# Optimization experiments

Hardware: AMD Instinct MI355X
Metric: run time of the kernel (lower is better)

Reference implementation:

```python
import jax, jax.numpy as jnp
import numpy as np

HIDDEN = 1024
HEADS = 16
CHUNK = 128
NEG_INF = -1e10  # matches source's -10000000000.0


def setup_inputs() -> dict:
    key = jax.random.key(0)
    k1, k2, k3 = jax.random.split(key, 3)
    B, S = 2, 4096
    x = jax.random.normal(k1, (B, S, HIDDEN), dtype=jnp.float32)
    w_qkv = jax.random.normal(k2, (HIDDEN, 3 * HIDDEN), dtype=jnp.float32) / np.sqrt(HIDDEN).astype(np.float32)
    w_out = jax.random.normal(k3, (HIDDEN, HIDDEN), dtype=jnp.float32) / np.sqrt(HIDDEN).astype(np.float32)
    return {"x": x, "w_qkv": w_qkv, "w_out": w_out}


def reference(x, w_qkv, w_out):
    B, S, _ = x.shape
    H, D = HEADS, HIDDEN // HEADS
    # fused qkv projection (flax Dense, no bias): [B,S,3,H,D]
    qkv = (x @ w_qkv).reshape(B, S, 3, H, D)
    q, k, v = qkv[:, :, 0], qkv[:, :, 1], qkv[:, :, 2]
    scale = jnp.sqrt(jnp.asarray(D, x.dtype))
    n_chunks = S // CHUNK
    # [n_chunks, B, CHUNK, H, D] query chunks; scan keeps only one chunk's
    # [B,H,CHUNK,S] score tensor live at a time (faithful to source's chunking).
    q_chunks = q.reshape(B, n_chunks, CHUNK, H, D).transpose(1, 0, 2, 3, 4)
    starts = jnp.arange(n_chunks) * CHUNK

    def step(carry, inp):
        qc, start = inp  # qc: [B,CHUNK,H,D]
        scores = jnp.einsum('bqhd,bkhd->bhqk', qc, k) / scale  # [B,H,CHUNK,S]
        causal = (jnp.arange(CHUNK)[:, None] + start) >= jnp.arange(S)[None, :]
        scores = jnp.where(causal[None, None], scores, NEG_INF)
        attn = jax.nn.softmax(scores, axis=-1)
        out_c = jnp.einsum('bhqk,bkhd->bqhd', attn, v).reshape(B, CHUNK, H * D)
        return carry, out_c

    _, outs = jax.lax.scan(step, None, (q_chunks, starts))  # [n,B,CHUNK,hidden]
    out = outs.transpose(1, 0, 2, 3).reshape(B, S, H * D)
    return out @ w_out
```

## Files before the change

kernel.cpp:

```cpp
#include <hip/hip_runtime.h>
#include <hip/hip_bf16.h>

#define SEQ 4096
#define BATCH 2
#define HEADS 16
#define DHEAD 64
#define HID 1024

typedef unsigned short ushort_t;
typedef unsigned int uint_t;
typedef __attribute__((ext_vector_type(8))) short short8;
typedef __attribute__((ext_vector_type(4))) float f32x4;
typedef __attribute__((ext_vector_type(16))) float f32x16;
typedef __attribute__((ext_vector_type(4))) uint_t u32x4;

__device__ __forceinline__ float exp2_fast(float x) {
  return __builtin_amdgcn_exp2f(x);
}

__device__ __forceinline__ float max3f(float a, float b, float c) {
  float r;
  asm("v_max3_f32 %0, %1, %2, %3" : "=v"(r) : "v"(a), "v"(b), "v"(c));
  return r;
}

__device__ __forceinline__ ushort_t f2b(float f) {
  unsigned u = __builtin_bit_cast(unsigned, f);
  unsigned r = 0x7fffu + ((u >> 16) & 1u);
  return (ushort_t)((u + r) >> 16);
}

__device__ __forceinline__ uint_t cvt_pk_bf16(float lo, float hi) {
  uint_t r;
  asm("v_cvt_pk_bf16_f32 %0, %1, %2" : "=v"(r) : "v"(lo), "v"(hi));
  return r;
}

__device__ __forceinline__ void permlane_swap(uint_t& a, uint_t& b) {
  asm("v_permlane32_swap_b32 %0, %1" : "+v"(a), "+v"(b));
}

__device__ __forceinline__ void gload16(const void* g, void* l) {
  __builtin_amdgcn_global_load_lds((const __attribute__((address_space(1))) void*)g,
                                   (__attribute__((address_space(3))) void*)l, 16, 0, 0);
}

__device__ __forceinline__ f32x4 mfma_bf16(short8 a, short8 b, f32x4 c) {
  return __builtin_amdgcn_mfma_f32_16x16x32_bf16(a, b, c, 0, 0, 0);
}

__device__ __forceinline__ f32x16 mfma32_bf16(short8 a, short8 b, f32x16 c) {
  return __builtin_amdgcn_mfma_f32_32x32x16_bf16(a, b, c, 0, 0, 0);
}

__global__ void cvt_kernel(const float* __restrict__ in, ushort_t* __restrict__ out, int n4) {
  int i = blockIdx.x * blockDim.x + threadIdx.x;
  if (i >= n4) return;
  float4 v = reinterpret_cast<const float4*>(in)[i];
  ushort4 o;
  o.x = f2b(v.x); o.y = f2b(v.y); o.z = f2b(v.z); o.w = f2b(v.w);
  reinterpret_cast<ushort4*>(out)[i] = o;
}

__global__ void transpose_cvt_kernel(const float* __restrict__ in, ushort_t* __restrict__ out,
                                     int rows, int cols) {
  __shared__ float tile[32][33];
  int tx = threadIdx.x & 31, ty = threadIdx.x >> 5;
  int r0 = blockIdx.y * 32, c0 = blockIdx.x * 32;
#pragma unroll
  for (int i = 0; i < 32; i += 8)
    tile[ty + i][tx] = in[(size_t)(r0 + ty + i) * cols + c0 + tx];
  __syncthreads();
#pragma unroll
  for (int i = 0; i < 32; i += 8)
    out[(size_t)(c0 + ty + i) * rows + r0 + tx] = f2b(tile[tx][ty + i]);
}

template <int MODE>
__global__ __launch_bounds__(256, 2)
void gemm_kernel(const ushort_t* __restrict__ A, const ushort_t* __restrict__ BT,
                 int M, int N, int K,
                 ushort_t* __restrict__ qg, ushort_t* __restrict__ kg,
                 ushort_t* __restrict__ vTg, float* __restrict__ outf) {
  __shared__ ushort_t lA[128 * 64];
  __shared__ ushort_t lB[128 * 64];
  int tid = threadIdx.x;
  int lane = tid & 63, w = tid >> 6;
  int m0 = blockIdx.x * 128, n0 = blockIdx.y * 128;
  int wr = (w >> 1) * 64, wc = (w & 1) * 64;
  int lr = lane & 15, lg = lane >> 4;

  const f32x4 z4 = {0.f, 0.f, 0.f, 0.f};
  f32x4 acc[4][4];
#pragma unroll
  for (int m = 0; m < 4; ++m)
#pragma unroll
    for (int n = 0; n < 4; ++n) acc[m][n] = z4;

  int ktiles = K >> 6;
  for (int kt = 0; kt < ktiles; ++kt) {
    int k0 = kt << 6;
#pragma unroll
    for (int i = 0; i < 4; ++i) {
      int c = i * 256 + tid;
      int row = c >> 3, cc = c & 7;
      gload16(A + (size_t)(m0 + row) * K + k0 + (cc ^ (row & 7)) * 8, lA + c * 8);
    }
#pragma unroll
    for (int i = 0; i < 4; ++i) {
      int c = i * 256 + tid;
      int row = c >> 3, cc = c & 7;
      gload16(BT + (size_t)(n0 + row) * K + k0 + (cc ^ (row & 7)) * 8, lB + c * 8);
    }
    __syncthreads();
#pragma unroll
    for (int kk = 0; kk < 2; ++kk) {
      short8 a[4], b[4];
#pragma unroll
      for (int m = 0; m < 4; ++m) {
        int row = wr + m * 16 + lr, cc = kk * 4 + lg;
        a[m] = *(const short8*)(lA + row * 64 + ((cc ^ (row & 7)) << 3));
      }
#pragma unroll
      for (int n = 0; n < 4; ++n) {
        int row = wc + n * 16 + lr, cc = kk * 4 + lg;
        b[n] = *(const short8*)(lB + row * 64 + ((cc ^ (row & 7)) << 3));
      }
      __builtin_amdgcn_s_setprio(1);
#pragma unroll
      for (int m = 0; m < 4; ++m)
#pragma unroll
        for (int n = 0; n < 4; ++n)
          acc[m][n] = mfma_bf16(a[m], b[n], acc[m][n]);
      __builtin_amdgcn_s_setprio(0);
    }
    __syncthreads();
  }

#pragma unroll
  for (int m = 0; m < 4; ++m)
#pragma unroll
    for (int n = 0; n < 4; ++n)
#pragma unroll
      for (int r = 0; r < 4; ++r) {
        int i = m0 + wr + m * 16 + lg * 4 + r;
        int j = n0 + wc + n * 16 + lr;
        float v = acc[m][n][r];
        if (MODE == 0) {
          int mat = j >> 10, rem = j & 1023;
          int h = rem >> 6, d = rem & 63;
          int b = i >> 12, s = i & 4095;
          int bh = b * HEADS + h;
          ushort_t val = f2b(mat == 0 ? v * 0.18033688f : v);
          if (mat == 0)      qg[((size_t)bh * SEQ + s) * DHEAD + d] = val;
          else if (mat == 1) kg[((size_t)bh * SEQ + s) * DHEAD + d] = val;
          else               vTg[((size_t)bh * DHEAD + d) * SEQ + s] = val;
        } else {
          outf[(size_t)i * N + j] = v;
        }
      }
}

struct QS {
  short8 qf[4];
  f32x16 o[2];
  float mrow, lsum;
};

__device__ __forceinline__ void attn_tile(int diag, int w, int l31, int hi, int lane,
                                          const ushort_t* lKc, const ushort_t* lVc, QS& st) {
  f32x16 s[4];
#pragma unroll
  for (int t = 0; t < 4; ++t)
#pragma unroll
    for (int r = 0; r < 16; ++r) s[t][r] = 0.f;

#pragma unroll
  for (int t = 0; t < 4; ++t) {
    int row = t * 32 + l31;
#pragma unroll
    for (int kb = 0; kb < 4; ++kb) {
      int cc = kb * 2 + hi;
      short8 kf = *(const short8*)(lKc + row * 64 + ((cc ^ (row & 7)) << 3));
      __builtin_amdgcn_s_setprio(1);
      s[t] = mfma32_bf16(kf, st.qf[kb], s[t]);
      __builtin_amdgcn_s_setprio(0);
    }
  }

  if (diag) {
    int q = w * 32 + l31;
#pragma unroll
    for (int t = 0; t < 4; ++t)
#pragma unroll
      for (int r = 0; r < 16; ++r)
        if (t * 32 + (r & 3) + 8 * (r >> 2) + 4 * hi > q) s[t][r] = -1e30f;
  }

  float mx = fmaxf(s[0][0], s[0][1]);
#pragma unroll
  for (int t = 0; t < 4; ++t)
#pragma unroll
    for (int r = (t == 0 ? 2 : 0); r < 16; r += 2)
      mx = max3f(mx, s[t][r], s[t][r + 1]);
  mx = fmaxf(mx, __shfl_xor(mx, 32));
  float mo = st.mrow;
  if (!__all(mx - mo <= 8.0f)) {
    float mn = fmaxf(mo, mx);
    float al = exp2_fast(mo - mn);
    st.mrow = mn;
    st.lsum *= al;
#pragma unroll
    for (int r = 0; r < 16; ++r) {
      float alo = __shfl(al, (r & 3) + 8 * (r >> 2) + 4 * hi);
      st.o[0][r] *= alo;
      st.o[1][r] *= alo;
    }
  }
  float mloc = st.mrow;
  float rsv[4];
#pragma unroll
  for (int t = 0; t < 4; ++t) {
    float a = 0.f;
#pragma unroll
    for (int r = 0; r < 16; ++r) {
      float p = exp2_fast(s[t][r] - mloc);
      s[t][r] = p;
      a += p;
    }
    rsv[t] = a;
  }
  float rs = (rsv[0] + rsv[1]) + (rsv[2] + rsv[3]);
  rs += __shfl_xor(rs, 32);
  st.lsum += rs;

  short8 pa[8];
#pragma unroll
  for (int t = 0; t < 4; ++t) {
    uint_t w0 = cvt_pk_bf16(s[t][0], s[t][1]);
    uint_t w1 = cvt_pk_bf16(s[t][2], s[t][3]);
    uint_t w2 = cvt_pk_bf16(s[t][4], s[t][5]);
    uint_t w3 = cvt_pk_bf16(s[t][6], s[t][7]);
    permlane_swap(w0, w2);
    permlane_swap(w1, w3);
    u32x4 f0 = {w0, w1, w2, w3};
    pa[2 * t] = __builtin_bit_cast(short8, f0);
    uint_t w4 = cvt_pk_bf16(s[t][8], s[t][9]);
    uint_t w5 = cvt_pk_bf16(s[t][10], s[t][11]);
    uint_t w6 = cvt_pk_bf16(s[t][12], s[t][13]);
    uint_t w7 = cvt_pk_bf16(s[t][14], s[t][15]);
    permlane_swap(w4, w6);
    permlane_swap(w5, w7);
    u32x4 f1 = {w4, w5, w6, w7};
    pa[2 * t + 1] = __builtin_bit_cast(short8, f1);
  }

#pragma unroll
  for (int nd = 0; nd < 2; ++nd) {
    int row = nd * 32 + l31;
#pragma unroll
    for (int kb = 0; kb < 8; ++kb) {
      int cc = kb * 2 + hi;
      short8 vf = *(const short8*)(lVc + row * 128 + ((cc ^ (row & 15)) << 3));
      __builtin_amdgcn_s_setprio(1);
      st.o[nd] = mfma32_bf16(pa[kb], vf, st.o[nd]);
      __builtin_amdgcn_s_setprio(0);
    }
  }
}

__device__ __forceinline__ void attn_epilogue(const QS& st, int q0, int bh,
                                              int w, int l31, int hi,
                                              ushort_t* __restrict__ og) {
  int b = bh >> 4, h = bh & 15;
#pragma unroll
  for (int r = 0; r < 16; ++r) {
    int qr = (r & 3) + 8 * (r >> 2) + 4 * hi;
    float ls = __shfl(st.lsum, qr);
    float inv = 1.0f / ls;
    int srow = q0 + w * 32 + qr;
#pragma unroll
    for (int nd = 0; nd < 2; ++nd) {
      int col = h * 64 + nd * 32 + l31;
      og[((size_t)b * SEQ + srow) * HID + col] = f2b(st.o[nd][r] * inv);
    }
  }
}

__global__ __launch_bounds__(256, 2)
void attn_kernel(const ushort_t* __restrict__ qg, const ushort_t* __restrict__ kg,
                 const ushort_t* __restrict__ vTg, ushort_t* __restrict__ og) {
  __shared__ ushort_t lK[2][128 * 64];
  __shared__ ushort_t lV[2][64 * 128];

  int bid = blockIdx.x;
  int wg = (bid & 7) * 64 + (bid >> 3);
  int bh = wg >> 4;
  int pair = wg & 15;
  int qtA = 31 - pair, qtB = pair;
  int q0A = qtA * 128, q0B = qtB * 128;
  const ushort_t* Q = qg + (size_t)bh * SEQ * DHEAD;
  const ushort_t* Kp = kg + (size_t)bh * SEQ * DHEAD;
  const ushort_t* Vt = vTg + (size_t)bh * DHEAD * SEQ;

  int tid = threadIdx.x, lane = tid & 63, w = tid >> 6;
  int l31 = lane & 31, hi = lane >> 5;

#pragma unroll
  for (int i = 0; i < 4; ++i) {
    int c = i * 256 + tid;
    int row = c >> 3, cc = c & 7;
    size_t qoff = (cc ^ (row & 7)) * 8;
    gload16(Q + (size_t)(q0A + row) * DHEAD + qoff, &lK[1][c * 8]);
    gload16(Q + (size_t)(q0B + row) * DHEAD + qoff, &lV[1][c * 8]);
    gload16(Kp + (size_t)row * DHEAD + qoff, &lK[0][c * 8]);
  }
#pragma unroll
  for (int i = 0; i < 4; ++i) {
    int c = i * 256 + tid;
    int d = c >> 4, cc = c & 15;
    gload16(Vt + (size_t)d * SEQ + (cc ^ (d & 15)) * 8, &lV[0][c * 8]);
  }
  __syncthreads();

  QS stA, stB;
  int qrow = w * 32 + l31;
#pragma unroll
  for (int kb = 0; kb < 4; ++kb) {
    int cc = kb * 2 + hi;
    int off = qrow * 64 + ((cc ^ (qrow & 7)) << 3);
    stA.qf[kb] = *(const short8*)(&lK[1][0] + off);
    stB.qf[kb] = *(const short8*)(&lV[1][0] + off);
  }
  asm volatile("s_waitcnt lgkmcnt(0)");
  __syncthreads();

  stA.mrow = -1e30f; stA.lsum = 0.f;
  stB.mrow = -1e30f; stB.lsum = 0.f;
#pragma unroll
  for (int nd = 0; nd < 2; ++nd)
#pragma unroll
    for (int r = 0; r < 16; ++r) { stA.o[nd][r] = 0.f; stB.o[nd][r] = 0.f; }

  for (int jt = 0; jt <= qtA; ++jt) {
    int cur = jt & 1, nxt = cur ^ 1;
    if (jt < qtA) {
      int j0n = (jt + 1) * 128;
#pragma unroll
      for (int i = 0; i < 4; ++i) {
        int c = i * 256 + tid;
        int row = c >> 3, cc = c & 7;
        gload16(Kp + (size_t)(j0n + row) * DHEAD + (cc ^ (row & 7)) * 8, &lK[nxt][c * 8]);
      }
#pragma unroll
      for (int i = 0; i < 4; ++i) {
        int c = i * 256 + tid;
        int d = c >> 4, cc = c & 15;
        gload16(Vt + (size_t)d * SEQ + j0n + (cc ^ (d & 15)) * 8, &lV[nxt][c * 8]);
      }
    }

    attn_tile(jt == qtA, w, l31, hi, lane, &lK[cur][0], &lV[cur][0], stA);
    if (jt <= qtB)
      attn_tile(jt == qtB, w, l31, hi, lane, &lK[cur][0], &lV[cur][0], stB);

    __syncthreads();
  }

  attn_epilogue(stA, q0A, bh, w, l31, hi, og);
  attn_epilogue(stB, q0B, bh, w, l31, hi, og);
}

extern "C" void kernel_launch(void* const* d_in, const int* in_sizes, int n_in,
                              void* d_out, int out_size, void* d_ws, size_t ws_size,
                              hipStream_t stream) {
  const float* x = (const float*)d_in[0];
  const float* wqkv = (const float*)d_in[1];
  const float* wout = (const float*)d_in[2];
  float* out = (float*)d_out;

  if (ws_size < 75497472u) return;

  char* ws = (char*)d_ws;
  ushort_t* xb    = (ushort_t*)(ws);
  ushort_t* wqkvT = (ushort_t*)(ws + 16777216);
  ushort_t* woutT = (ushort_t*)(ws + 23068672);
  ushort_t* qgb   = (ushort_t*)(ws + 25165824);
  ushort_t* kgb   = (ushort_t*)(ws + 41943040);
  ushort_t* vTb   = (ushort_t*)(ws + 58720256);
  ushort_t* ob    = xb;

  cvt_kernel<<<dim3(8192), dim3(256), 0, stream>>>(x, xb, 2097152);
  transpose_cvt_kernel<<<dim3(96, 32), dim3(256), 0, stream>>>(wqkv, wqkvT, 1024, 3072);
  transpose_cvt_kernel<<<dim3(32, 32), dim3(256), 0, stream>>>(wout, woutT, 1024, 1024);
  gemm_kernel<0><<<dim3(64, 24), dim3(256), 0, stream>>>(xb, wqkvT, 8192, 3072, 1024,
                                                         qgb, kgb, vTb, nullptr);
  attn_kernel<<<dim3(512), dim3(256), 0, stream>>>(qgb, kgb, vTb, ob);
  gemm_kernel<1><<<dim3(64, 8), dim3(256), 0, stream>>>(ob, woutT, 8192, 1024, 1024,
                                                        nullptr, nullptr, nullptr, out);
}
```

Before: 217.6 us.

## Split paired query tiles into one block per tile with single-buffered V

Each block previously handled a balanced pair of query tiles (long and short) sharing K/V loads. Now each block processes a single query tile, doubling the grid, with heaviest tiles scheduled first and heads grouped per XCD. V is single-buffered and loaded at the start of each iteration, with an added barrier between QK/softmax and PV to cut LDS use. This trades K/V reuse across two query tiles and V prefetch overlap for more independent blocks and less LDS.

```diff
diff --git a/kernel.cpp b/kernel.cpp
--- a/kernel.cpp
+++ b/kernel.cpp
@@ -167,8 +167,8 @@
   float mrow, lsum;
 };
 
-__device__ __forceinline__ void attn_tile(int diag, int w, int l31, int hi, int lane,
-                                          const ushort_t* lKc, const ushort_t* lVc, QS& st) {
+__device__ __forceinline__ void attn_qk_sm(int diag, int w, int l31, int hi, int lane,
+                                           const ushort_t* lKc, QS& st, short8 (&pa)[8]) {
   f32x16 s[4];
 #pragma unroll
   for (int t = 0; t < 4; ++t)
@@ -234,7 +234,6 @@
   rs += __shfl_xor(rs, 32);
   st.lsum += rs;
 
-  short8 pa[8];
 #pragma unroll
   for (int t = 0; t < 4; ++t) {
     uint_t w0 = cvt_pk_bf16(s[t][0], s[t][1]);
@@ -254,7 +253,10 @@
     u32x4 f1 = {w4, w5, w6, w7};
     pa[2 * t + 1] = __builtin_bit_cast(short8, f1);
   }
-
+}
+
+__device__ __forceinline__ void attn_pv(const ushort_t* lVc, int l31, int hi,
+                                        const short8 (&pa)[8], QS& st) {
 #pragma unroll
   for (int nd = 0; nd < 2; ++nd) {
     int row = nd * 32 + l31;
@@ -291,14 +293,13 @@
 void attn_kernel(const ushort_t* __restrict__ qg, const ushort_t* __restrict__ kg,
                  const ushort_t* __restrict__ vTg, ushort_t* __restrict__ og) {
   __shared__ ushort_t lK[2][128 * 64];
-  __shared__ ushort_t lV[2][64 * 128];
+  __shared__ ushort_t lV[64 * 128];
 
   int bid = blockIdx.x;
-  int wg = (bid & 7) * 64 + (bid >> 3);
-  int bh = wg >> 4;
-  int pair = wg & 15;
-  int qtA = 31 - pair, qtB = pair;
-  int q0A = qtA * 128, q0B = qtB * 128;
+  int xcd = bid & 7, idx = bid >> 3;
+  int bh = xcd * 4 + (idx & 3);
+  int qt = 31 - (idx >> 2);
+  int q0 = qt * 128;
   const ushort_t* Q = qg + (size_t)bh * SEQ * DHEAD;
   const ushort_t* Kp = kg + (size_t)bh * SEQ * DHEAD;
   const ushort_t* Vt = vTg + (size_t)bh * DHEAD * SEQ;
@@ -310,41 +311,37 @@
   for (int i = 0; i < 4; ++i) {
     int c = i * 256 + tid;
     int row = c >> 3, cc = c & 7;
-    size_t qoff = (cc ^ (row & 7)) * 8;
-    gload16(Q + (size_t)(q0A + row) * DHEAD + qoff, &lK[1][c * 8]);
-    gload16(Q + (size_t)(q0B + row) * DHEAD + qoff, &lV[1][c * 8]);
-    gload16(Kp + (size_t)row * DHEAD + qoff, &lK[0][c * 8]);
-  }
-#pragma unroll
-  for (int i = 0; i < 4; ++i) {
-    int c = i * 256 + tid;
-    int d = c >> 4, cc = c & 15;
-    gload16(Vt + (size_t)d * SEQ + (cc ^ (d & 15)) * 8, &lV[0][c * 8]);
+    size_t off = (cc ^ (row & 7)) * 8;
+    gload16(Q + (size_t)(q0 + row) * DHEAD + off, &lV[c * 8]);
+    gload16(Kp + (size_t)row * DHEAD + off, &lK[0][c * 8]);
   }
   __syncthreads();
 
-  QS stA, stB;
+  QS st;
   int qrow = w * 32 + l31;
 #pragma unroll
   for (int kb = 0; kb < 4; ++kb) {
     int cc = kb * 2 + hi;
-    int off = qrow * 64 + ((cc ^ (qrow & 7)) << 3);
-    stA.qf[kb] = *(const short8*)(&lK[1][0] + off);
-    stB.qf[kb] = *(const short8*)(&lV[1][0] + off);
+    st.qf[kb] = *(const short8*)(&lV[0] + qrow * 64 + ((cc ^ (qrow & 7)) << 3));
   }
   asm volatile("s_waitcnt lgkmcnt(0)");
   __syncthreads();
 
-  stA.mrow = -1e30f; stA.lsum = 0.f;
-  stB.mrow = -1e30f; stB.lsum = 0.f;
+  st.mrow = -1e30f; st.lsum = 0.f;
 #pragma unroll
   for (int nd = 0; nd < 2; ++nd)
 #pragma unroll
-    for (int r = 0; r < 16; ++r) { stA.o[nd][r] = 0.f; stB.o[nd][r] = 0.f; }
-
-  for (int jt = 0; jt <= qtA; ++jt) {
+    for (int r = 0; r < 16; ++r) st.o[nd][r] = 0.f;
+
+  for (int jt = 0; jt <= qt; ++jt) {
     int cur = jt & 1, nxt = cur ^ 1;
-    if (jt < qtA) {
+#pragma unroll
+    for (int i = 0; i < 4; ++i) {
+      int c = i * 256 + tid;
+      int d = c >> 4, cc = c & 15;
+      gload16(Vt + (size_t)d * SEQ + jt * 128 + (cc ^ (d & 15)) * 8, &lV[c * 8]);
+    }
+    if (jt < qt) {
       int j0n = (jt + 1) * 128;
 #pragma unroll
       for (int i = 0; i < 4; ++i) {
@@ -352,23 +349,17 @@
         int row = c >> 3, cc = c & 7;
         gload16(Kp + (size_t)(j0n + row) * DHEAD + (cc ^ (row & 7)) * 8, &lK[nxt][c * 8]);
       }
-#pragma unroll
-      for (int i = 0; i < 4; ++i) {
-        int c = i * 256 + tid;
-        int d = c >> 4, cc = c & 15;
-        gload16(Vt + (size_t)d * SEQ + j0n + (cc ^ (d & 15)) * 8, &lV[nxt][c * 8]);
-      }
-    }
-
-    attn_tile(jt == qtA, w, l31, hi, lane, &lK[cur][0], &lV[cur][0], stA);
-    if (jt <= qtB)
-      attn_tile(jt == qtB, w, l31, hi, lane, &lK[cur][0], &lV[cur][0], stB);
+    }
+
+    short8 pa[8];
+    attn_qk_sm(jt == qt, w, l31, hi, lane, &lK[cur][0], st, pa);
 
     __syncthreads();
-  }
-
-  attn_epilogue(stA, q0A, bh, w, l31, hi, og);
-  attn_epilogue(stB, q0B, bh, w, l31, hi, og);
+    attn_pv(&lV[0], l31, hi, pa, st);
+    __syncthreads();
+  }
+
+  attn_epilogue(st, q0, bh, w, l31, hi, og);
 }
 
 extern "C" void kernel_launch(void* const* d_in, const int* in_sizes, int n_in,
@@ -395,7 +386,7 @@
   transpose_cvt_kernel<<<dim3(32, 32), dim3(256), 0, stream>>>(wout, woutT, 1024, 1024);
   gemm_kernel<0><<<dim3(64, 24), dim3(256), 0, stream>>>(xb, wqkvT, 8192, 3072, 1024,
                                                          qgb, kgb, vTb, nullptr);
-  attn_kernel<<<dim3(512), dim3(256), 0, stream>>>(qgb, kgb, vTb, ob);
+  attn_kernel<<<dim3(1024), dim3(256), 0, stream>>>(qgb, kgb, vTb, ob);
   gemm_kernel<1><<<dim3(64, 8), dim3(256), 0, stream>>>(ob, woutT, 8192, 1024, 1024,
                                                         nullptr, nullptr, nullptr, out);
 }
```

New measurement: 218.3 us. No clear change (+0.3%).
